# Kernel optimization log

Measured on AMD Instinct MI355X. Metric: run time of the kernel, lower is better.

Reference implementation:

```python
import jax, jax.numpy as jnp
import numpy as np
from jax import lax


def setup_inputs() -> dict:
    key = jax.random.key(0)
    k1, k2, k3, k4 = jax.random.split(key, 4)
    N, T = 4096, 64          # num_nodes, tokens per node
    V, H, L = 30000, 256, 2  # vocab, hidden size, LSTM layers
    data = jax.random.randint(k1, (N, T), 0, V, dtype=jnp.int64)
    embed = jax.random.uniform(k2, (V, H), jnp.float32, -0.1, 0.1)
    Wx = jax.random.normal(k3, (L, H, 4 * H), jnp.float32) * 0.05
    Wh = jax.random.normal(k4, (L, H, 4 * H), jnp.float32) * 0.05
    b = jnp.zeros((L, 4 * H), jnp.float32)
    return {"data": data, "embed": embed, "Wx": Wx, "Wh": Wh, "b": b}


def _stacked_lstm_last(tok, Wx, Wh, b):
    # tok: [N, T, H]; Wx/Wh: [L, H, 4H]; b: [L, 4H]
    L, H = Wx.shape[0], Wx.shape[1]
    N = tok.shape[0]
    xs = jnp.swapaxes(tok, 0, 1)  # [T, N, H] -- scan over time, batched over nodes
    c0 = jnp.zeros((L, N, H), tok.dtype)
    h0 = jnp.zeros((L, N, H), tok.dtype)

    def step(carry, x_t):
        c, h = carry
        inp = x_t
        new_c, new_h = [], []
        for l in range(L):  # small fixed layer loop
            z = inp @ Wx[l] + h[l] @ Wh[l] + b[l]  # [N, 4H]
            i, f, g, o = jnp.split(z, 4, axis=-1)   # flax gate order i, f, g, o
            i, f, o = jax.nn.sigmoid(i), jax.nn.sigmoid(f), jax.nn.sigmoid(o)
            g = jnp.tanh(g)
            cl = f * c[l] + i * g
            hl = o * jnp.tanh(cl)
            new_c.append(cl)
            new_h.append(hl)
            inp = hl  # top layer output feeds next layer
        return (jnp.stack(new_c), jnp.stack(new_h)), None

    (_, hF), _ = lax.scan(step, (c0, h0), xs)
    # result[-1] in the original is the top-layer output at the final step,
    # which equals the final top-layer hidden state.
    return hF[-1]  # [N, H]


def reference(data, embed, Wx, Wh, b):
    tok = embed[data]  # [N, T, H] embedding lookup
    return _stacked_lstm_last(tok, Wx, Wh, b)
```

## Files before the change

kernel.cpp:

```cpp
#include <hip/hip_runtime.h>
#include <hip/hip_bf16.h>

#define TT 64
#define HH 256
#define GG 1024

typedef _Float16 f16;
typedef __attribute__((ext_vector_type(8))) _Float16 f16x8;
typedef __attribute__((ext_vector_type(4))) _Float16 f16x4;
typedef __attribute__((ext_vector_type(4))) float f32x4;

__device__ __forceinline__ float exp2_(float x) { return __builtin_amdgcn_exp2f(x); }
__device__ __forceinline__ float sig_(float x) {
    return __builtin_amdgcn_rcpf(1.0f + exp2_(-1.44269504f * x));
}
__device__ __forceinline__ float tanh_(float x) {
    return 1.0f - 2.0f * __builtin_amdgcn_rcpf(1.0f + exp2_(2.88539008f * x));
}
__device__ __forceinline__ float sigp_(float x) { return 1.0f / (1.0f + __expf(-x)); }
__device__ __forceinline__ float tanhp_(float x) {
    x = fminf(fmaxf(x, -15.0f), 15.0f);
    float e = __expf(-2.0f * x);
    return (1.0f - e) / (1.0f + e);
}

__global__ void pack_weights(const float* __restrict__ Wx, const float* __restrict__ Wh,
                             f16* __restrict__ Wp) {
    int t = blockIdx.x * 256 + threadIdx.x;
    int lane = t & 63;
    int nt = (t >> 6) & 63;
    int kk = (t >> 12) & 15;
    int l = t >> 16;
    int n = nt * 16 + (lane & 15);
    int kbase = kk * 32 + 8 * (lane >> 4);
    const float* src = (kbase < 256) ? (Wx + (size_t)l * HH * GG + (size_t)kbase * GG + n)
                                     : (Wh + (size_t)l * HH * GG + (size_t)(kbase - 256) * GG + n);
    f16x8 v;
#pragma unroll
    for (int j = 0; j < 8; ++j) v[j] = (f16)src[(size_t)j * GG];
    *(f16x8*)(Wp + (size_t)t * 8) = v;
}

__global__ __launch_bounds__(512) void embw_gemm(
    const float* __restrict__ embed, const float* __restrict__ bias,
    const f16* __restrict__ Wp, f16* __restrict__ embW, int vocab)
{
    __shared__ f16 a_lds[32 * HH];
    const int tid = threadIdx.x;
    const int lane = tid & 63;
    const int w = tid >> 6;
    const int arow = lane & 15;
    const int g4 = lane >> 4;
    const int r0 = blockIdx.x * 32;

#pragma unroll
    for (int i = 0; i < 4; ++i) {
        int chunk = tid + i * 512;
        int row = chunk >> 6;
        int c4 = chunk & 63;
        int grow = r0 + row; if (grow >= vocab) grow = vocab - 1;
        float4 v = *(const float4*)(embed + (size_t)grow * HH + c4 * 4);
        int idx = row * HH + ((c4 * 4) ^ ((row & 7) << 3));
        *(f16x4*)&a_lds[idx] = (f16x4){(f16)v.x, (f16)v.y, (f16)v.z, (f16)v.w};
    }
    __syncthreads();

    float breg[8];
#pragma unroll
    for (int tt = 0; tt < 8; ++tt) breg[tt] = bias[(w * 8 + tt) * 16 + arow];

    f32x4 acc[2][8];
#pragma unroll
    for (int mt = 0; mt < 2; ++mt)
#pragma unroll
        for (int tt = 0; tt < 8; ++tt)
            acc[mt][tt] = (f32x4){breg[tt], breg[tt], breg[tt], breg[tt]};

    const f16* wl = Wp + (size_t)lane * 8;
#pragma unroll 2
    for (int kk = 0; kk < 8; ++kk) {
        int sw = (kk * 32 + g4 * 8) ^ ((arow & 7) << 3);
        f16x8 a0 = *(const f16x8*)&a_lds[arow * HH + sw];
        f16x8 a1 = *(const f16x8*)&a_lds[(arow + 16) * HH + sw];
        const f16* wkk = wl + (size_t)kk * 64 * 64 * 8;
#pragma unroll
        for (int tt = 0; tt < 8; ++tt) {
            f16x8 b = *(const f16x8*)(wkk + (size_t)(w * 8 + tt) * 64 * 8);
            acc[0][tt] = __builtin_amdgcn_mfma_f32_16x16x32_f16(a0, b, acc[0][tt], 0, 0, 0);
            acc[1][tt] = __builtin_amdgcn_mfma_f32_16x16x32_f16(a1, b, acc[1][tt], 0, 0, 0);
        }
    }

#pragma unroll
    for (int mt = 0; mt < 2; ++mt)
#pragma unroll
        for (int tt = 0; tt < 8; ++tt) {
            int nt = w * 8 + tt;
            int cw = (nt >> 1) & 7;
            int ctt = ((nt >> 4) << 1) | (nt & 1);
#pragma unroll
            for (int r = 0; r < 4; ++r) {
                int row = r0 + mt * 16 + g4 * 4 + r;
                if (row < vocab)
                    embW[(size_t)row * GG + cw * 128 + arow * 8 + ctt] = (f16)acc[mt][tt][r];
            }
        }
}

#define NB2 32
#define LDH 264

__global__ __launch_bounds__(512, 1) void lstm_rec2(
    const int* __restrict__ data, const float* __restrict__ bias,
    const f16* __restrict__ embW, const f16* __restrict__ Wp,
    float* __restrict__ out)
{
    __shared__ f16 h0s[NB2 * LDH];
    __shared__ f16 h1s[NB2 * LDH];
    __shared__ int toks[NB2 * TT];

    const int tid = threadIdx.x;
    const int lane = tid & 63;
    const int w = tid >> 6;
    const int arow = lane & 15;
    const int g4 = lane >> 4;
    const int n0 = blockIdx.x * NB2;

    for (int i = tid; i < NB2 * LDH; i += 512) { h0s[i] = (f16)0; h1s[i] = (f16)0; }
    for (int i = tid; i < NB2 * TT; i += 512) toks[i] = data[n0 * TT + i];

    float breg1[8];
#pragma unroll
    for (int tt = 0; tt < 8; ++tt) {
        int col = (tt >> 1) * 256 + w * 32 + (tt & 1) * 16 + arow;
        breg1[tt] = bias[GG + col];
    }

    float c0[16], c1[16];
#pragma unroll
    for (int i = 0; i < 16; ++i) { c0[i] = 0.0f; c1[i] = 0.0f; }

    const f16* wl0 = Wp + (size_t)8 * 64 * 64 * 8 + (size_t)lane * 8;
    const f16* wl1 = Wp + (size_t)16 * 64 * 64 * 8 + (size_t)lane * 8;
    const int zoff = w * 128 + arow * 8;

    __syncthreads();

#pragma unroll 1
    for (int t = 0; t < TT; ++t) {
        f32x4 acc[2][8];
#pragma unroll
        for (int mt = 0; mt < 2; ++mt) {
            f16x8 zf0, zf1, zf2, zf3;
            {
                int nb = mt * 16 + g4 * 4;
                int t0 = toks[(nb + 0) * TT + t];
                int t1 = toks[(nb + 1) * TT + t];
                int t2 = toks[(nb + 2) * TT + t];
                int t3 = toks[(nb + 3) * TT + t];
                zf0 = *(const f16x8*)(embW + (size_t)t0 * GG + zoff);
                zf1 = *(const f16x8*)(embW + (size_t)t1 * GG + zoff);
                zf2 = *(const f16x8*)(embW + (size_t)t2 * GG + zoff);
                zf3 = *(const f16x8*)(embW + (size_t)t3 * GG + zoff);
            }
#pragma unroll
            for (int tt = 0; tt < 8; ++tt) {
                acc[mt][tt][0] = (float)zf0[tt];
                acc[mt][tt][1] = (float)zf1[tt];
                acc[mt][tt][2] = (float)zf2[tt];
                acc[mt][tt][3] = (float)zf3[tt];
            }
        }

#pragma unroll 2
        for (int kk = 0; kk < 8; ++kk) {
            int k0 = kk * 32 + 8 * g4;
            f16x8 a0 = *(const f16x8*)&h0s[arow * LDH + k0];
            f16x8 a1 = *(const f16x8*)&h0s[(arow + 16) * LDH + k0];
            const f16* wkk = wl0 + (size_t)kk * 64 * 64 * 8;
#pragma unroll
            for (int tt = 0; tt < 8; ++tt) {
                int nt = (tt >> 1) * 16 + w * 2 + (tt & 1);
                f16x8 b = *(const f16x8*)(wkk + (size_t)nt * 64 * 8);
                acc[0][tt] = __builtin_amdgcn_mfma_f32_16x16x32_f16(a0, b, acc[0][tt], 0, 0, 0);
                acc[1][tt] = __builtin_amdgcn_mfma_f32_16x16x32_f16(a1, b, acc[1][tt], 0, 0, 0);
            }
        }
        __syncthreads();

#pragma unroll
        for (int mt = 0; mt < 2; ++mt)
#pragma unroll
            for (int sub = 0; sub < 2; ++sub)
#pragma unroll
                for (int r = 0; r < 4; ++r) {
                    int node = mt * 16 + g4 * 4 + r;
                    float i_ = sig_(acc[mt][0 + sub][r]);
                    float f_ = sig_(acc[mt][2 + sub][r]);
                    float g_ = tanh_(acc[mt][4 + sub][r]);
                    float o_ = sig_(acc[mt][6 + sub][r]);
                    int ci = mt * 8 + sub * 4 + r;
                    float c = fmaf(f_, c0[ci], i_ * g_);
                    c0[ci] = c;
                    int u = w * 32 + sub * 16 + arow;
                    h0s[node * LDH + u] = (f16)(o_ * tanh_(c));
                }
        __syncthreads();

        f32x4 acc1[2][8];
#pragma unroll
        for (int mt = 0; mt < 2; ++mt)
#pragma unroll
            for (int tt = 0; tt < 8; ++tt)
                acc1[mt][tt] = (f32x4){breg1[tt], breg1[tt], breg1[tt], breg1[tt]};

#pragma unroll 2
        for (int kk = 0; kk < 16; ++kk) {
            const f16* asrc = (kk < 8) ? h0s : h1s;
            int k0 = (kk & 7) * 32 + 8 * g4;
            f16x8 a0 = *(const f16x8*)&asrc[arow * LDH + k0];
            f16x8 a1 = *(const f16x8*)&asrc[(arow + 16) * LDH + k0];
            const f16* wkk = wl1 + (size_t)kk * 64 * 64 * 8;
#pragma unroll
            for (int tt = 0; tt < 8; ++tt) {
                int nt = (tt >> 1) * 16 + w * 2 + (tt & 1);
                f16x8 b = *(const f16x8*)(wkk + (size_t)nt * 64 * 8);
                acc1[0][tt] = __builtin_amdgcn_mfma_f32_16x16x32_f16(a0, b, acc1[0][tt], 0, 0, 0);
                acc1[1][tt] = __builtin_amdgcn_mfma_f32_16x16x32_f16(a1, b, acc1[1][tt], 0, 0, 0);
            }
        }
        __syncthreads();

#pragma unroll
        for (int mt = 0; mt < 2; ++mt)
#pragma unroll
            for (int sub = 0; sub < 2; ++sub)
#pragma unroll
                for (int r = 0; r < 4; ++r) {
                    int node = mt * 16 + g4 * 4 + r;
                    float i_ = sig_(acc1[mt][0 + sub][r]);
                    float f_ = sig_(acc1[mt][2 + sub][r]);
                    float g_ = tanh_(acc1[mt][4 + sub][r]);
                    float o_ = sig_(acc1[mt][6 + sub][r]);
                    int ci = mt * 8 + sub * 4 + r;
                    float c = fmaf(f_, c1[ci], i_ * g_);
                    c1[ci] = c;
                    int u = w * 32 + sub * 16 + arow;
                    h1s[node * LDH + u] = (f16)(o_ * tanh_(c));
                }
    }
    __syncthreads();

    for (int i = tid; i < NB2 * HH; i += 512) {
        int n = i >> 8, k = i & 255;
        out[(size_t)(n0 + n) * HH + k] = (float)h1s[n * LDH + k];
    }
}

__global__ void convert_embed(const float* __restrict__ e, f16* __restrict__ o, int n8) {
    int i = blockIdx.x * 256 + threadIdx.x;
    if (i >= n8) return;
    size_t p = (size_t)i * 8;
    float4 a = *(const float4*)(e + p);
    float4 b = *(const float4*)(e + p + 4);
    f16x8 v = { (f16)a.x, (f16)a.y, (f16)a.z, (f16)a.w,
                (f16)b.x, (f16)b.y, (f16)b.z, (f16)b.w };
    *(f16x8*)(o + p) = v;
}

#define FB 32
#define FTH 512
#define FLD 264
__device__ __forceinline__ void fb_layer_step(
    const f16 (*bx)[FLD], f16 (*bh)[FLD], const f16* __restrict__ wlayer,
    const float* breg_l, float* c_l, int lane, int w)
{
    f32x4 acc[2][8];
#pragma unroll
    for (int mt = 0; mt < 2; ++mt)
#pragma unroll
        for (int tt = 0; tt < 8; ++tt) {
            float b = breg_l[tt];
            acc[mt][tt] = (f32x4){b, b, b, b};
        }
    const int arow = lane & 15;
    const int koff = 8 * (lane >> 4);
    const f16* wl = wlayer + (size_t)lane * 8;
#pragma unroll 2
    for (int kk = 0; kk < 16; ++kk) {
        int k0 = (kk & 7) * 32 + koff;
        const f16(*src)[FLD] = (kk < 8) ? bx : (const f16(*)[FLD])bh;
        f16x8 a0 = *(const f16x8*)&src[arow][k0];
        f16x8 a1 = *(const f16x8*)&src[arow + 16][k0];
        const f16* wkk = wl + (size_t)kk * 64 * 64 * 8;
#pragma unroll
        for (int tt = 0; tt < 8; ++tt) {
            int nt = (tt >> 1) * 16 + w * 2 + (tt & 1);
            f16x8 b = *(const f16x8*)(wkk + (size_t)nt * 64 * 8);
            acc[0][tt] = __builtin_amdgcn_mfma_f32_16x16x32_f16(a0, b, acc[0][tt], 0, 0, 0);
            acc[1][tt] = __builtin_amdgcn_mfma_f32_16x16x32_f16(a1, b, acc[1][tt], 0, 0, 0);
        }
    }
    __syncthreads();
#pragma unroll
    for (int mt = 0; mt < 2; ++mt)
#pragma unroll
        for (int sub = 0; sub < 2; ++sub) {
            f32x4 iv = acc[mt][0 + sub], fv = acc[mt][2 + sub];
            f32x4 gv = acc[mt][4 + sub], ov = acc[mt][6 + sub];
#pragma unroll
            for (int r = 0; r < 4; ++r) {
                float i_ = sigp_(iv[r]), f_ = sigp_(fv[r]), g_ = tanhp_(gv[r]), o_ = sigp_(ov[r]);
                int ci = mt * 8 + sub * 4 + r;
                float c = fmaf(f_, c_l[ci], i_ * g_);
                c_l[ci] = c;
                int node = mt * 16 + (lane >> 4) * 4 + r;
                int unit = w * 32 + sub * 16 + (lane & 15);
                bh[node][unit] = (f16)(o_ * tanhp_(c));
            }
        }
    __syncthreads();
}

__global__ __launch_bounds__(FTH, 2) void lstm_mfma_fb(
    const int* __restrict__ data, const float* __restrict__ bias,
    const f16* __restrict__ emb, const f16* __restrict__ Wp,
    float* __restrict__ out, int vocab)
{
    __shared__ f16 x_lds[FB][FLD];
    __shared__ f16 h0_lds[FB][FLD];
    __shared__ f16 h1_lds[FB][FLD];
    const int tid = threadIdx.x;
    const int lane = tid & 63;
    const int w = tid >> 6;
    const int n0 = blockIdx.x * FB;
    for (int i = tid; i < FB * FLD; i += FTH) {
        (&h0_lds[0][0])[i] = (f16)0.0f; (&h1_lds[0][0])[i] = (f16)0.0f;
    }
    float breg[2][8];
#pragma unroll
    for (int l = 0; l < 2; ++l)
#pragma unroll
        for (int tt = 0; tt < 8; ++tt) {
            int col = (tt >> 1) * 256 + w * 32 + (tt & 1) * 16 + (lane & 15);
            breg[l][tt] = bias[l * GG + col];
        }
    float cst[2][16];
#pragma unroll
    for (int i = 0; i < 32; ++i) (&cst[0][0])[i] = 0.0f;
    __syncthreads();
    const f16* Wp0 = Wp;
    const f16* Wp1 = Wp + (size_t)16 * 64 * 64 * 8;
    for (int t = 0; t < TT; ++t) {
        {
            int n = tid >> 4;
            int cg = (tid & 15) * 16;
            int row = data[(n0 + n) * TT + t];
            row = min(max(row, 0), vocab - 1);
            const f16* src = emb + (size_t)row * HH + cg;
            *(f16x8*)&x_lds[n][cg] = *(const f16x8*)src;
            *(f16x8*)&x_lds[n][cg + 8] = *(const f16x8*)(src + 8);
        }
        __syncthreads();
        fb_layer_step(x_lds, h0_lds, Wp0, breg[0], cst[0], lane, w);
        fb_layer_step((const f16(*)[FLD])h0_lds, h1_lds, Wp1, breg[1], cst[1], lane, w);
    }
    for (int i = tid; i < FB * HH; i += FTH) {
        int n = i >> 8, k = i & 255;
        out[(size_t)(n0 + n) * HH + k] = (float)h1_lds[n][k];
    }
}

extern "C" void kernel_launch(void* const* d_in, const int* in_sizes, int n_in,
                              void* d_out, int out_size, void* d_ws, size_t ws_size,
                              hipStream_t stream) {
    const int* data = (const int*)d_in[0];
    const float* embed = (const float*)d_in[1];
    const float* Wx = (const float*)d_in[2];
    const float* Wh = (const float*)d_in[3];
    const float* bias = (const float*)d_in[4];
    float* out = (float*)d_out;
    const int vocab = in_sizes[1] / HH;
    const int nNodes = in_sizes[0] / TT;

    const size_t wp_bytes = (size_t)2 * 16 * 64 * 64 * 8 * 2;
    const size_t embw_bytes = (size_t)vocab * GG * 2;
    const size_t emb16_bytes = (size_t)vocab * HH * 2;

    if (ws_size >= embw_bytes + wp_bytes) {
        f16* embW = (f16*)d_ws;
        f16* Wp = (f16*)((char*)d_ws + embw_bytes);
        pack_weights<<<dim3(512), dim3(256), 0, stream>>>(Wx, Wh, Wp);
        embw_gemm<<<dim3((vocab + 31) / 32), dim3(512), 0, stream>>>(embed, bias, Wp, embW, vocab);
        lstm_rec2<<<dim3(nNodes / NB2), dim3(512), 0, stream>>>(data, bias, embW, Wp, out);
        return;
    }
    f16* emb_h = (f16*)d_ws;
    f16* Wp = (f16*)((char*)d_ws + emb16_bytes);
    int n8 = in_sizes[1] / 8;
    convert_embed<<<dim3((n8 + 255) / 256), dim3(256), 0, stream>>>(embed, emb_h, n8);
    pack_weights<<<dim3(512), dim3(256), 0, stream>>>(Wx, Wh, Wp);
    lstm_mfma_fb<<<dim3(nNodes / FB), dim3(FTH), 0, stream>>>(data, bias, emb_h, Wp, out, vocab);
}
```

Measured before the change: 1.324 ms.

## Double-buffer recurrent weight chunks into LDS via async global_load_lds

Recurrent weight tiles are now streamed into two shared-memory buffers with global_load_lds, instead of each wave reading them straight from global memory. The next half-chunk is prefetched while MFMAs consume the current one, so weight-fetch latency can overlap with compute. The cost is a barrier after every half-chunk, 64KB of extra LDS, and full unrolling of the k-loops. There is also a possible hazard: the LDS write may not be complete at the barrier without an explicit vmcnt wait.

```diff
diff --git a/kernel.cpp b/kernel.cpp
--- a/kernel.cpp
+++ b/kernel.cpp
@@ -110,11 +110,36 @@
 #define NB2 32
 #define LDH 264
 
+#define STAGE(GBASE, LBUF)                                                        \
+    {                                                                             \
+        const f16* gsrc_ = (GBASE) + (size_t)tid * 8;                             \
+        f16* ldst_ = (LBUF) + w * 512;                                            \
+        _Pragma("unroll")                                                         \
+        for (int i_ = 0; i_ < 4; ++i_)                                            \
+            __builtin_amdgcn_global_load_lds(                                     \
+                (__attribute__((address_space(1))) void*)(f16*)(gsrc_ + (size_t)i_ * 4096), \
+                (__attribute__((address_space(3))) void*)(ldst_ + (size_t)i_ * 4096),       \
+                16, 0, 0);                                                        \
+    }
+
+#define CHUNK_COMPUTE(ACC, BUF, A0, A1, H)                                        \
+    _Pragma("unroll")                                                             \
+    for (int ttl_ = 0; ttl_ < 4; ++ttl_) {                                        \
+        int ntl_ = (ttl_ >> 1) * 16 + w * 2 + (ttl_ & 1);                         \
+        f16x8 b_ = *(const f16x8*)&(BUF)[ntl_ * 512 + lane * 8];                  \
+        (ACC)[0][(H) * 4 + ttl_] = __builtin_amdgcn_mfma_f32_16x16x32_f16(        \
+            (A0), b_, (ACC)[0][(H) * 4 + ttl_], 0, 0, 0);                         \
+        (ACC)[1][(H) * 4 + ttl_] = __builtin_amdgcn_mfma_f32_16x16x32_f16(        \
+            (A1), b_, (ACC)[1][(H) * 4 + ttl_], 0, 0, 0);                         \
+    }
+
 __global__ __launch_bounds__(512, 1) void lstm_rec2(
     const int* __restrict__ data, const float* __restrict__ bias,
     const f16* __restrict__ embW, const f16* __restrict__ Wp,
     float* __restrict__ out)
 {
+    __shared__ __align__(16) f16 bufA[16384];
+    __shared__ __align__(16) f16 bufB[16384];
     __shared__ f16 h0s[NB2 * LDH];
     __shared__ f16 h1s[NB2 * LDH];
     __shared__ int toks[NB2 * TT];
@@ -140,10 +165,13 @@
 #pragma unroll
     for (int i = 0; i < 16; ++i) { c0[i] = 0.0f; c1[i] = 0.0f; }
 
-    const f16* wl0 = Wp + (size_t)8 * 64 * 64 * 8 + (size_t)lane * 8;
-    const f16* wl1 = Wp + (size_t)16 * 64 * 64 * 8 + (size_t)lane * 8;
+    const f16* W_L0 = Wp + (size_t)8 * 32768;
+    const f16* W_L1 = Wp + (size_t)16 * 32768;
     const int zoff = w * 128 + arow * 8;
 
+    __syncthreads();
+
+    STAGE(W_L0, bufA)
     __syncthreads();
 
 #pragma unroll 1
@@ -172,21 +200,19 @@
             }
         }
 
-#pragma unroll 2
+#pragma unroll
         for (int kk = 0; kk < 8; ++kk) {
+            STAGE(W_L0 + (size_t)kk * 32768 + 16384, bufB)
             int k0 = kk * 32 + 8 * g4;
             f16x8 a0 = *(const f16x8*)&h0s[arow * LDH + k0];
             f16x8 a1 = *(const f16x8*)&h0s[(arow + 16) * LDH + k0];
-            const f16* wkk = wl0 + (size_t)kk * 64 * 64 * 8;
-#pragma unroll
-            for (int tt = 0; tt < 8; ++tt) {
-                int nt = (tt >> 1) * 16 + w * 2 + (tt & 1);
-                f16x8 b = *(const f16x8*)(wkk + (size_t)nt * 64 * 8);
-                acc[0][tt] = __builtin_amdgcn_mfma_f32_16x16x32_f16(a0, b, acc[0][tt], 0, 0, 0);
-                acc[1][tt] = __builtin_amdgcn_mfma_f32_16x16x32_f16(a1, b, acc[1][tt], 0, 0, 0);
-            }
-        }
-        __syncthreads();
+            CHUNK_COMPUTE(acc, bufA, a0, a1, 0)
+            __syncthreads();
+            if (kk < 7) { STAGE(W_L0 + (size_t)(kk + 1) * 32768, bufA) }
+            else        { STAGE(W_L1, bufA) }
+            CHUNK_COMPUTE(acc, bufB, a0, a1, 1)
+            __syncthreads();
+        }
 
 #pragma unroll
         for (int mt = 0; mt < 2; ++mt)
@@ -214,22 +240,20 @@
             for (int tt = 0; tt < 8; ++tt)
                 acc1[mt][tt] = (f32x4){breg1[tt], breg1[tt], breg1[tt], breg1[tt]};
 
-#pragma unroll 2
+#pragma unroll
         for (int kk = 0; kk < 16; ++kk) {
             const f16* asrc = (kk < 8) ? h0s : h1s;
+            STAGE(W_L1 + (size_t)kk * 32768 + 16384, bufB)
             int k0 = (kk & 7) * 32 + 8 * g4;
             f16x8 a0 = *(const f16x8*)&asrc[arow * LDH + k0];
             f16x8 a1 = *(const f16x8*)&asrc[(arow + 16) * LDH + k0];
-            const f16* wkk = wl1 + (size_t)kk * 64 * 64 * 8;
-#pragma unroll
-            for (int tt = 0; tt < 8; ++tt) {
-                int nt = (tt >> 1) * 16 + w * 2 + (tt & 1);
-                f16x8 b = *(const f16x8*)(wkk + (size_t)nt * 64 * 8);
-                acc1[0][tt] = __builtin_amdgcn_mfma_f32_16x16x32_f16(a0, b, acc1[0][tt], 0, 0, 0);
-                acc1[1][tt] = __builtin_amdgcn_mfma_f32_16x16x32_f16(a1, b, acc1[1][tt], 0, 0, 0);
-            }
-        }
-        __syncthreads();
+            CHUNK_COMPUTE(acc1, bufA, a0, a1, 0)
+            __syncthreads();
+            if (kk < 15) { STAGE(W_L1 + (size_t)(kk + 1) * 32768, bufA) }
+            else         { STAGE(W_L0, bufA) }
+            CHUNK_COMPUTE(acc1, bufB, a0, a1, 1)
+            __syncthreads();
+        }
 
 #pragma unroll
         for (int mt = 0; mt < 2; ++mt)
```

After: 4.555 ms. +244.1%, slower.

## Split recurrent LSTM block across 16 waves and double-buffer layer-1 hidden state

Applied to the files above, without the earlier changes.

Each block now runs 1024 threads, so each wave handles one 16-node M-tile instead of two. That halves the accumulator registers per wave and doubles the number of waves available to hide MFMA and weight-load latency. The layer-1 hidden state is double-buffered, which removes one __syncthreads per timestep. The embedding-gate contribution is now added after the MFMA loop instead of being used to initialise the accumulators. Every wave still loads the full B weight fragments, so global and L2 weight traffic per block doubles.

```diff
diff --git a/kernel.cpp b/kernel.cpp
--- a/kernel.cpp
+++ b/kernel.cpp
@@ -109,151 +109,152 @@
 
 #define NB2 32
 #define LDH 264
-
-__global__ __launch_bounds__(512, 1) void lstm_rec2(
+#define RTH 1024
+
+__global__ __launch_bounds__(RTH, 1) void lstm_rec2(
     const int* __restrict__ data, const float* __restrict__ bias,
     const f16* __restrict__ embW, const f16* __restrict__ Wp,
     float* __restrict__ out)
 {
     __shared__ f16 h0s[NB2 * LDH];
-    __shared__ f16 h1s[NB2 * LDH];
+    __shared__ f16 h1s[2][NB2 * LDH];
     __shared__ int toks[NB2 * TT];
 
     const int tid = threadIdx.x;
     const int lane = tid & 63;
     const int w = tid >> 6;
+    const int wq = w & 7;
+    const int mt = w >> 3;
     const int arow = lane & 15;
     const int g4 = lane >> 4;
     const int n0 = blockIdx.x * NB2;
 
-    for (int i = tid; i < NB2 * LDH; i += 512) { h0s[i] = (f16)0; h1s[i] = (f16)0; }
-    for (int i = tid; i < NB2 * TT; i += 512) toks[i] = data[n0 * TT + i];
+    for (int i = tid; i < NB2 * LDH; i += RTH) {
+        h0s[i] = (f16)0; h1s[0][i] = (f16)0; h1s[1][i] = (f16)0;
+    }
+    for (int i = tid; i < NB2 * TT; i += RTH) toks[i] = data[n0 * TT + i];
 
     float breg1[8];
 #pragma unroll
     for (int tt = 0; tt < 8; ++tt) {
-        int col = (tt >> 1) * 256 + w * 32 + (tt & 1) * 16 + arow;
+        int col = (tt >> 1) * 256 + wq * 32 + (tt & 1) * 16 + arow;
         breg1[tt] = bias[GG + col];
     }
 
-    float c0[16], c1[16];
-#pragma unroll
-    for (int i = 0; i < 16; ++i) { c0[i] = 0.0f; c1[i] = 0.0f; }
+    float c0[8], c1[8];
+#pragma unroll
+    for (int i = 0; i < 8; ++i) { c0[i] = 0.0f; c1[i] = 0.0f; }
 
     const f16* wl0 = Wp + (size_t)8 * 64 * 64 * 8 + (size_t)lane * 8;
     const f16* wl1 = Wp + (size_t)16 * 64 * 64 * 8 + (size_t)lane * 8;
-    const int zoff = w * 128 + arow * 8;
+    const int zoff = wq * 128 + arow * 8;
+    const int abase = (mt * 16 + arow) * LDH;
+
+    int cur1 = 0;
 
     __syncthreads();
 
 #pragma unroll 1
     for (int t = 0; t < TT; ++t) {
-        f32x4 acc[2][8];
-#pragma unroll
-        for (int mt = 0; mt < 2; ++mt) {
-            f16x8 zf0, zf1, zf2, zf3;
-            {
-                int nb = mt * 16 + g4 * 4;
-                int t0 = toks[(nb + 0) * TT + t];
-                int t1 = toks[(nb + 1) * TT + t];
-                int t2 = toks[(nb + 2) * TT + t];
-                int t3 = toks[(nb + 3) * TT + t];
-                zf0 = *(const f16x8*)(embW + (size_t)t0 * GG + zoff);
-                zf1 = *(const f16x8*)(embW + (size_t)t1 * GG + zoff);
-                zf2 = *(const f16x8*)(embW + (size_t)t2 * GG + zoff);
-                zf3 = *(const f16x8*)(embW + (size_t)t3 * GG + zoff);
-            }
-#pragma unroll
-            for (int tt = 0; tt < 8; ++tt) {
-                acc[mt][tt][0] = (float)zf0[tt];
-                acc[mt][tt][1] = (float)zf1[tt];
-                acc[mt][tt][2] = (float)zf2[tt];
-                acc[mt][tt][3] = (float)zf3[tt];
-            }
-        }
+        f16x8 zf0, zf1, zf2, zf3;
+        {
+            int nb = mt * 16 + g4 * 4;
+            int t0 = toks[(nb + 0) * TT + t];
+            int t1 = toks[(nb + 1) * TT + t];
+            int t2 = toks[(nb + 2) * TT + t];
+            int t3 = toks[(nb + 3) * TT + t];
+            zf0 = *(const f16x8*)(embW + (size_t)t0 * GG + zoff);
+            zf1 = *(const f16x8*)(embW + (size_t)t1 * GG + zoff);
+            zf2 = *(const f16x8*)(embW + (size_t)t2 * GG + zoff);
+            zf3 = *(const f16x8*)(embW + (size_t)t3 * GG + zoff);
+        }
+
+        f32x4 acc[8];
+#pragma unroll
+        for (int tt = 0; tt < 8; ++tt)
+            acc[tt] = (f32x4){0.0f, 0.0f, 0.0f, 0.0f};
 
 #pragma unroll 2
         for (int kk = 0; kk < 8; ++kk) {
             int k0 = kk * 32 + 8 * g4;
-            f16x8 a0 = *(const f16x8*)&h0s[arow * LDH + k0];
-            f16x8 a1 = *(const f16x8*)&h0s[(arow + 16) * LDH + k0];
+            f16x8 a0 = *(const f16x8*)&h0s[abase + k0];
             const f16* wkk = wl0 + (size_t)kk * 64 * 64 * 8;
 #pragma unroll
             for (int tt = 0; tt < 8; ++tt) {
-                int nt = (tt >> 1) * 16 + w * 2 + (tt & 1);
+                int nt = (tt >> 1) * 16 + wq * 2 + (tt & 1);
                 f16x8 b = *(const f16x8*)(wkk + (size_t)nt * 64 * 8);
-                acc[0][tt] = __builtin_amdgcn_mfma_f32_16x16x32_f16(a0, b, acc[0][tt], 0, 0, 0);
-                acc[1][tt] = __builtin_amdgcn_mfma_f32_16x16x32_f16(a1, b, acc[1][tt], 0, 0, 0);
-            }
+                acc[tt] = __builtin_amdgcn_mfma_f32_16x16x32_f16(a0, b, acc[tt], 0, 0, 0);
+            }
+        }
+
+#pragma unroll
+        for (int tt = 0; tt < 8; ++tt) {
+            acc[tt][0] += (float)zf0[tt];
+            acc[tt][1] += (float)zf1[tt];
+            acc[tt][2] += (float)zf2[tt];
+            acc[tt][3] += (float)zf3[tt];
         }
         __syncthreads();
 
 #pragma unroll
-        for (int mt = 0; mt < 2; ++mt)
-#pragma unroll
-            for (int sub = 0; sub < 2; ++sub)
-#pragma unroll
-                for (int r = 0; r < 4; ++r) {
-                    int node = mt * 16 + g4 * 4 + r;
-                    float i_ = sig_(acc[mt][0 + sub][r]);
-                    float f_ = sig_(acc[mt][2 + sub][r]);
-                    float g_ = tanh_(acc[mt][4 + sub][r]);
-                    float o_ = sig_(acc[mt][6 + sub][r]);
-                    int ci = mt * 8 + sub * 4 + r;
-                    float c = fmaf(f_, c0[ci], i_ * g_);
-                    c0[ci] = c;
-                    int u = w * 32 + sub * 16 + arow;
-                    h0s[node * LDH + u] = (f16)(o_ * tanh_(c));
-                }
+        for (int sub = 0; sub < 2; ++sub)
+#pragma unroll
+            for (int r = 0; r < 4; ++r) {
+                int node = mt * 16 + g4 * 4 + r;
+                float i_ = sig_(acc[0 + sub][r]);
+                float f_ = sig_(acc[2 + sub][r]);
+                float g_ = tanh_(acc[4 + sub][r]);
+                float o_ = sig_(acc[6 + sub][r]);
+                int ci = sub * 4 + r;
+                float c = fmaf(f_, c0[ci], i_ * g_);
+                c0[ci] = c;
+                int u = wq * 32 + sub * 16 + arow;
+                h0s[node * LDH + u] = (f16)(o_ * tanh_(c));
+            }
         __syncthreads();
 
-        f32x4 acc1[2][8];
-#pragma unroll
-        for (int mt = 0; mt < 2; ++mt)
-#pragma unroll
-            for (int tt = 0; tt < 8; ++tt)
-                acc1[mt][tt] = (f32x4){breg1[tt], breg1[tt], breg1[tt], breg1[tt]};
-
+        f32x4 acc1[8];
+#pragma unroll
+        for (int tt = 0; tt < 8; ++tt)
+            acc1[tt] = (f32x4){breg1[tt], breg1[tt], breg1[tt], breg1[tt]};
+
+        const f16* h1cur = h1s[cur1];
 #pragma unroll 2
         for (int kk = 0; kk < 16; ++kk) {
-            const f16* asrc = (kk < 8) ? h0s : h1s;
+            const f16* asrc = (kk < 8) ? h0s : h1cur;
             int k0 = (kk & 7) * 32 + 8 * g4;
-            f16x8 a0 = *(const f16x8*)&asrc[arow * LDH + k0];
-            f16x8 a1 = *(const f16x8*)&asrc[(arow + 16) * LDH + k0];
+            f16x8 a0 = *(const f16x8*)&asrc[abase + k0];
             const f16* wkk = wl1 + (size_t)kk * 64 * 64 * 8;
 #pragma unroll
             for (int tt = 0; tt < 8; ++tt) {
-                int nt = (tt >> 1) * 16 + w * 2 + (tt & 1);
+                int nt = (tt >> 1) * 16 + wq * 2 + (tt & 1);
                 f16x8 b = *(const f16x8*)(wkk + (size_t)nt * 64 * 8);
-                acc1[0][tt] = __builtin_amdgcn_mfma_f32_16x16x32_f16(a0, b, acc1[0][tt], 0, 0, 0);
-                acc1[1][tt] = __builtin_amdgcn_mfma_f32_16x16x32_f16(a1, b, acc1[1][tt], 0, 0, 0);
-            }
-        }
-        __syncthreads();
-
-#pragma unroll
-        for (int mt = 0; mt < 2; ++mt)
-#pragma unroll
-            for (int sub = 0; sub < 2; ++sub)
-#pragma unroll
-                for (int r = 0; r < 4; ++r) {
-                    int node = mt * 16 + g4 * 4 + r;
-                    float i_ = sig_(acc1[mt][0 + sub][r]);
-                    float f_ = sig_(acc1[mt][2 + sub][r]);
-                    float g_ = tanh_(acc1[mt][4 + sub][r]);
-                    float o_ = sig_(acc1[mt][6 + sub][r]);
-                    int ci = mt * 8 + sub * 4 + r;
-                    float c = fmaf(f_, c1[ci], i_ * g_);
-                    c1[ci] = c;
-                    int u = w * 32 + sub * 16 + arow;
-                    h1s[node * LDH + u] = (f16)(o_ * tanh_(c));
-                }
-    }
-    __syncthreads();
-
-    for (int i = tid; i < NB2 * HH; i += 512) {
+                acc1[tt] = __builtin_amdgcn_mfma_f32_16x16x32_f16(a0, b, acc1[tt], 0, 0, 0);
+            }
+        }
+
+#pragma unroll
+        for (int sub = 0; sub < 2; ++sub)
+#pragma unroll
+            for (int r = 0; r < 4; ++r) {
+                int node = mt * 16 + g4 * 4 + r;
+                float i_ = sig_(acc1[0 + sub][r]);
+                float f_ = sig_(acc1[2 + sub][r]);
+                float g_ = tanh_(acc1[4 + sub][r]);
+                float o_ = sig_(acc1[6 + sub][r]);
+                int ci = sub * 4 + r;
+                float c = fmaf(f_, c1[ci], i_ * g_);
+                c1[ci] = c;
+                int u = wq * 32 + sub * 16 + arow;
+                h1s[cur1 ^ 1][node * LDH + u] = (f16)(o_ * tanh_(c));
+            }
+        cur1 ^= 1;
+    }
+    __syncthreads();
+
+    for (int i = tid; i < NB2 * HH; i += RTH) {
         int n = i >> 8, k = i & 255;
-        out[(size_t)(n0 + n) * HH + k] = (float)h1s[n * LDH + k];
+        out[(size_t)(n0 + n) * HH + k] = (float)h1s[cur1][n * LDH + k];
     }
 }
 
@@ -392,7 +393,7 @@
         f16* Wp = (f16*)((char*)d_ws + embw_bytes);
         pack_weights<<<dim3(512), dim3(256), 0, stream>>>(Wx, Wh, Wp);
         embw_gemm<<<dim3((vocab + 31) / 32), dim3(512), 0, stream>>>(embed, bias, Wp, embW, vocab);
-        lstm_rec2<<<dim3(nNodes / NB2), dim3(512), 0, stream>>>(data, bias, embW, Wp, out);
+        lstm_rec2<<<dim3(nNodes / NB2), dim3(RTH), 0, stream>>>(data, bias, embW, Wp, out);
         return;
     }
     f16* emb_h = (f16*)d_ws;
```

After: 1.847 ms. 1.4x slower.
